# Kernel tuning notes

Measured on AMD Instinct MI355X. Metric: run time of the kernel, lower is better.

The kernel has to match this reference:

```python
import jax, jax.numpy as jnp
import numpy as np

WINDOW = 11
SIGMA = 1.5
C_IN = 3
PAD = WINDOW // 2
ALPHA_CHARB, ALPHA_MSE, ALPHA_SSIM = 0.3, 0.1, 0.6
EPS = 1e-6
C1 = (0.01 * 1) ** 2
C2 = (0.03 * 1) ** 2


def _gaussian_kernel():
    # 1D gaussian -> outer product -> depthwise weight [C, 1, K, K]
    x = np.arange(-(WINDOW // 2), WINDOW // 2 + 1, dtype=np.float32)
    w = np.exp(-0.5 * x * x / (SIGMA * SIGMA))
    w = w / w.sum()
    k2d = np.outer(w, w).astype(np.float32)  # [K, K]
    return jnp.asarray(np.tile(k2d[None, None], (C_IN, 1, 1, 1)))  # [C,1,K,K]

_KERNEL = _gaussian_kernel()


def _gauss_filter(x):
    # depthwise conv, NCHW / OIHW, SAME-style padding of K//2
    return jax.lax.conv_general_dilated(
        x, _KERNEL,
        window_strides=(1, 1),
        padding=[(PAD, PAD), (PAD, PAD)],
        dimension_numbers=('NCHW', 'OIHW', 'NCHW'),
        feature_group_count=C_IN,
    )


def setup_inputs() -> dict:
    key = jax.random.key(0)
    k1, k2 = jax.random.split(key)
    shape = (16, 3, 512, 512)
    pred = jax.random.uniform(k1, shape, dtype=jnp.float32)
    target = jax.random.uniform(k2, shape, dtype=jnp.float32)
    return {"pred": pred, "target": target}


def reference(pred, target):
    # SSIM map
    mu_x = _gauss_filter(pred)
    mu_y = _gauss_filter(target)
    sigma2_x = _gauss_filter(pred * pred) - mu_x * mu_x
    sigma2_y = _gauss_filter(target * target) - mu_y * mu_y
    sigma_xy = _gauss_filter(pred * target) - mu_x * mu_y
    A1 = 2.0 * mu_x * mu_y + C1
    A2 = 2.0 * sigma_xy + C2
    B1 = mu_x * mu_x + mu_y * mu_y + C1
    B2 = sigma2_x + sigma2_y + C2
    ssim = (A1 / B1) * (A2 / B2)

    diff = pred - target
    charb = jnp.sqrt(diff * diff + EPS * EPS)
    mse = diff * diff * 20.0
    ssim_loss = 1.0 - ssim
    return ALPHA_CHARB * charb + ALPHA_MSE * mse + ALPHA_SSIM * ssim_loss
```

## Files before the change

### kernel.cpp

```cpp
#include <hip/hip_runtime.h>


#define IMG    512
#define RAD    5
#define KW     11
#define STRH   64
#define NSTEP  (STRH + 2 * RAD)
#define ROWE   74
#define PLANE  (IMG * IMG)

#define C1F  1e-4f
#define C2F  9e-4f
#define EPS2 1e-12f

#define W0 0.00102838f
#define W1 0.00759876f
#define W2 0.03600076f
#define W3 0.10936067f
#define W4 0.21300537f
#define W5 0.26601297f

__global__ __launch_bounds__(256, 2)
void CombinedLossSSIMCharbMSE_81372450390186_kernel(
    const float* __restrict__ pred,
    const float* __restrict__ target,
    float* __restrict__ out)
{
    const float GW[KW] = {W0, W1, W2, W3, W4, W5, W4, W3, W2, W1, W0};

    __shared__ float2 rb[8 * ROWE];

    const int lane = threadIdx.x & 63;
    const int wav  = threadIdx.x >> 6;
    const int wid  = (blockIdx.x << 2) | wav;
    const int plane = wid >> 6;
    const int tile  = (wid >> 3) & 7;
    const int strip = wid & 7;
    const int col0 = strip << 6;
    const int row0 = tile << 6;
    const int pbase = plane * PLANE;

    const int  cA  = col0 - RAD + lane;
    const bool okA = (cA >= 0) & (cA < IMG);
    const int  cAc = min(max(cA, 0), IMG - 1);
    const int  cB  = col0 + 59 + lane;
    const bool okB = cB < IMG;
    const int  cBc = min(cB, IMG - 1);
    const bool doB = lane < 10;

    float hrx[KW], hry[KW], hrs[KW], hrp[KW], dring[KW];
#pragma unroll
    for (int s = 0; s < KW; ++s) {
        hrx[s] = 0.f; hry[s] = 0.f; hrs[s] = 0.f; hrp[s] = 0.f; dring[s] = 0.f;
    }

    float pAr = 0.f, tAr = 0.f, pBr = 0.f, tBr = 0.f;

#define LOAD_ROW(rr) do {                                                   \
        const int _base = pbase + (rr) * IMG;                               \
        pAr = pred[_base + cAc];   pAr = okA ? pAr : 0.f;                   \
        tAr = target[_base + cAc]; tAr = okA ? tAr : 0.f;                   \
        if (doB) {                                                          \
            pBr = pred[_base + cBc];   pBr = okB ? pBr : 0.f;               \
            tBr = target[_base + cBc]; tBr = okB ? tBr : 0.f;               \
        }                                                                   \
    } while (0)

#define COMMIT(par) do {                                                    \
        float2* _w = &rb[(((wav) << 1) | (par)) * ROWE];                    \
        _w[lane] = make_float2(pAr, tAr);                                   \
        if (doB) _w[64 + lane] = make_float2(pBr, tBr);                     \
        __builtin_amdgcn_wave_barrier();        \
    } while (0)

#define TAPS(uu, par) do {                                                  \
        const float2* _rd = &rb[(((wav) << 1) | (par)) * ROWE];             \
        float _hx = 0.f, _hy = 0.f, _hs = 0.f, _hp = 0.f;                   \
        float2 _c5 = make_float2(0.f, 0.f);                                 \
        _Pragma("unroll")                                                   \
        for (int _d = 0; _d < KW; ++_d) {                                   \
            const float2 _t = _rd[lane + _d];                               \
            if (_d == RAD) _c5 = _t;                                        \
            const float _w = GW[_d];                                        \
            _hx = fmaf(_w, _t.x, _hx);                                      \
            _hy = fmaf(_w, _t.y, _hy);                                      \
            _hs = fmaf(_w, fmaf(_t.x, _t.x, _t.y * _t.y), _hs);             \
            _hp = fmaf(_w, _t.x * _t.y, _hp);                               \
        }                                                                   \
        hrx[uu] = _hx; hry[uu] = _hy; hrs[uu] = _hs; hrp[uu] = _hp;         \
        dring[uu] = _c5.x - _c5.y;       \
    } while (0)

#define ZERO_H(uu) do {                                                     \
        hrx[uu] = 0.f; hry[uu] = 0.f; hrs[uu] = 0.f; hrp[uu] = 0.f;         \
    } while (0)

#define FINALIZE(uu, oo) do {                                               \
        float _vx = 0.f, _vy = 0.f, _vs = 0.f, _vp = 0.f;                   \
        _Pragma("unroll")                                                   \
        for (int _s = 0; _s < KW; ++_s) {                                   \
            const float _w = GW[((uu) - _s + KW) % KW];                     \
            _vx = fmaf(_w, hrx[_s], _vx);                                   \
            _vy = fmaf(_w, hry[_s], _vy);                                   \
            _vs = fmaf(_w, hrs[_s], _vs);                                   \
            _vp = fmaf(_w, hrp[_s], _vp);                                   \
        }                                                                   \
        const float _mxy = _vx * _vy;                                       \
        const float _mu2 = fmaf(_vx, _vx, _vy * _vy);                       \
        const float _A1 = fmaf(2.f, _mxy, C1F);                             \
        const float _A2 = fmaf(2.f, _vp - _mxy, C2F);                       \
        const float _B1 = _mu2 + C1F;                                       \
        const float _B2 = (_vs - _mu2) + C2F;                               \
        const float _ssim = (_A1 * _A2) * __builtin_amdgcn_rcpf(_B1 * _B2); \
        const float _dd = dring[((uu) + 6) % KW];     \
        const float _ch = __builtin_amdgcn_sqrtf(fmaf(_dd, _dd, EPS2));     \
        out[pbase + (oo) * IMG + col0 + lane] =                             \
            fmaf(0.3f, _ch, fmaf(2.0f, _dd * _dd, 0.6f * (1.f - _ssim)));   \
    } while (0)

    if (row0 > 0) LOAD_ROW(row0 - RAD);

#define STEP_PRO(uu) do {                                                   \
        const bool _inr = (row0 - RAD + (uu)) >= 0;       \
        if (_inr) COMMIT((uu) & 1);                                         \
        if ((row0 - RAD + (uu) + 1) >= 0) LOAD_ROW(row0 - RAD + (uu) + 1);  \
        if (_inr) TAPS(uu, (uu) & 1); else ZERO_H(uu);                      \
    } while (0)

    STEP_PRO(0); STEP_PRO(1); STEP_PRO(2); STEP_PRO(3); STEP_PRO(4);
    STEP_PRO(5); STEP_PRO(6); STEP_PRO(7); STEP_PRO(8); STEP_PRO(9);
    STEP_PRO(10);
    FINALIZE(10, row0);

    for (int k = 1; k <= 5; ++k) {
        const int rnext = row0 - RAD + k * KW + 1;
        const int obase = row0 + k * KW - 10;
        const int kp = k & 1;
#define STEP_FULL(uu) do {                                                  \
        COMMIT(kp ^ ((uu) & 1));                                            \
        LOAD_ROW(rnext + (uu));                                             \
        TAPS(uu, kp ^ ((uu) & 1));                                          \
        FINALIZE(uu, obase + (uu));                                         \
    } while (0)
        STEP_FULL(0); STEP_FULL(1); STEP_FULL(2); STEP_FULL(3);
        STEP_FULL(4); STEP_FULL(5); STEP_FULL(6); STEP_FULL(7);
        STEP_FULL(8); STEP_FULL(9); STEP_FULL(10);
#undef STEP_FULL
    }

#define STEP_EPI(uu) do {                                                   \
        const bool _inr = (row0 + 61 + (uu)) < IMG;       \
        if (_inr) COMMIT((uu) & 1);             \
        if (((uu) < 7) && (row0 + 62 + (uu)) < IMG)                         \
            LOAD_ROW(row0 + 62 + (uu));                                     \
        if (_inr) TAPS(uu, (uu) & 1); else ZERO_H(uu);                      \
        FINALIZE(uu, row0 + 56 + (uu));                                     \
    } while (0)

    STEP_EPI(0); STEP_EPI(1); STEP_EPI(2); STEP_EPI(3);
    STEP_EPI(4); STEP_EPI(5); STEP_EPI(6); STEP_EPI(7);
#undef STEP_EPI
#undef STEP_PRO
#undef FINALIZE
#undef ZERO_H
#undef TAPS
#undef COMMIT
#undef LOAD_ROW
}

extern "C" void kernel_launch(void* const* d_in, const int* in_sizes, int n_in,
                              void* d_out, int out_size, void* d_ws, size_t ws_size,
                              hipStream_t stream) {
    const float* pred = (const float*)d_in[0];
    const float* target = (const float*)d_in[1];
    float* out = (float*)d_out;
    const int planes = in_sizes[0] / PLANE;

    dim3 grid(planes * 16);
    CombinedLossSSIMCharbMSE_81372450390186_kernel<<<grid, dim3(256), 0, stream>>>(
        pred, target, out);
}
```

Baseline: 183.8 us.

## Prefetch input rows two steps ahead with a single LDS row buffer

Result: faster. 164.7 us (-10.4%).

```diff
diff --git a/kernel.cpp b/kernel.cpp
--- a/kernel.cpp
+++ b/kernel.cpp
@@ -5,7 +5,6 @@
 #define RAD    5
 #define KW     11
 #define STRH   64
-#define NSTEP  (STRH + 2 * RAD)
 #define ROWE   74
 #define PLANE  (IMG * IMG)
 
@@ -28,7 +27,7 @@
 {
     const float GW[KW] = {W0, W1, W2, W3, W4, W5, W4, W3, W2, W1, W0};
 
-    __shared__ float2 rb[8 * ROWE];
+    __shared__ float2 rb[4 * ROWE];
 
     const int lane = threadIdx.x & 63;
     const int wav  = threadIdx.x >> 6;
@@ -48,38 +47,41 @@
     const int  cBc = min(cB, IMG - 1);
     const bool doB = lane < 10;
 
+    const int wb = wav * ROWE;
+
     float hrx[KW], hry[KW], hrs[KW], hrp[KW], dring[KW];
 #pragma unroll
     for (int s = 0; s < KW; ++s) {
         hrx[s] = 0.f; hry[s] = 0.f; hrs[s] = 0.f; hrp[s] = 0.f; dring[s] = 0.f;
     }
 
-    float pAr = 0.f, tAr = 0.f, pBr = 0.f, tBr = 0.f;
+    float pA0 = 0.f, tA0 = 0.f, pB0 = 0.f, tB0 = 0.f;
+    float pA1 = 0.f, tA1 = 0.f, pB1 = 0.f, tB1 = 0.f;
 
-#define LOAD_ROW(rr) do {                                                   \
-        const int _base = pbase + (rr) * IMG;                               \
-        pAr = pred[_base + cAc];   pAr = okA ? pAr : 0.f;                   \
-        tAr = target[_base + cAc]; tAr = okA ? tAr : 0.f;                   \
+#define LOADR(ss, rr) do {                                                  \
+        const int _b = pbase + (rr) * IMG;                                  \
+        pA##ss = pred[_b + cAc];                                            \
+        tA##ss = target[_b + cAc];                                          \
         if (doB) {                                                          \
-            pBr = pred[_base + cBc];   pBr = okB ? pBr : 0.f;               \
-            tBr = target[_base + cBc]; tBr = okB ? tBr : 0.f;               \
+            pB##ss = pred[_b + cBc];                                        \
+            tB##ss = target[_b + cBc];                                      \
         }                                                                   \
     } while (0)
 
-#define COMMIT(par) do {                                                    \
-        float2* _w = &rb[(((wav) << 1) | (par)) * ROWE];                    \
-        _w[lane] = make_float2(pAr, tAr);                                   \
-        if (doB) _w[64 + lane] = make_float2(pBr, tBr);                     \
+#define COMMITR(ss) do {                                                    \
+        rb[wb + lane] =                                                     \
+            make_float2(okA ? pA##ss : 0.f, okA ? tA##ss : 0.f);            \
+        if (doB) rb[wb + 64 + lane] =                                       \
+            make_float2(okB ? pB##ss : 0.f, okB ? tB##ss : 0.f);            \
         __builtin_amdgcn_wave_barrier();        \
     } while (0)
 
-#define TAPS(uu, par) do {                                                  \
-        const float2* _rd = &rb[(((wav) << 1) | (par)) * ROWE];             \
+#define TAPS(uu) do {                                                       \
         float _hx = 0.f, _hy = 0.f, _hs = 0.f, _hp = 0.f;                   \
         float2 _c5 = make_float2(0.f, 0.f);                                 \
         _Pragma("unroll")                                                   \
         for (int _d = 0; _d < KW; ++_d) {                                   \
-            const float2 _t = _rd[lane + _d];                               \
+            const float2 _t = rb[wb + lane + _d];                           \
             if (_d == RAD) _c5 = _t;                                        \
             const float _w = GW[_d];                                        \
             _hx = fmaf(_w, _t.x, _hx);                                      \
@@ -118,54 +120,69 @@
             fmaf(0.3f, _ch, fmaf(2.0f, _dd * _dd, 0.6f * (1.f - _ssim)));   \
     } while (0)
 
-    if (row0 > 0) LOAD_ROW(row0 - RAD);
+    if (row0 > 0) { LOADR(0, row0 - 5); LOADR(1, row0 - 4); }
 
-#define STEP_PRO(uu) do {                                                   \
+#define STEP_PRO(uu, ss) do {                                               \
         const bool _inr = (row0 - RAD + (uu)) >= 0;       \
-        if (_inr) COMMIT((uu) & 1);                                         \
-        if ((row0 - RAD + (uu) + 1) >= 0) LOAD_ROW(row0 - RAD + (uu) + 1);  \
-        if (_inr) TAPS(uu, (uu) & 1); else ZERO_H(uu);                      \
+        if (_inr) COMMITR(ss);                                              \
+        if ((row0 - 3 + (uu)) >= 0) LOADR(ss, row0 - 3 + (uu));             \
+        if (_inr) TAPS(uu); else ZERO_H(uu);                                \
     } while (0)
 
-    STEP_PRO(0); STEP_PRO(1); STEP_PRO(2); STEP_PRO(3); STEP_PRO(4);
-    STEP_PRO(5); STEP_PRO(6); STEP_PRO(7); STEP_PRO(8); STEP_PRO(9);
-    STEP_PRO(10);
+    STEP_PRO(0, 0); STEP_PRO(1, 1); STEP_PRO(2, 0); STEP_PRO(3, 1);
+    STEP_PRO(4, 0); STEP_PRO(5, 1); STEP_PRO(6, 0); STEP_PRO(7, 1);
+    STEP_PRO(8, 0); STEP_PRO(9, 1); STEP_PRO(10, 0);
     FINALIZE(10, row0);
 
-    for (int k = 1; k <= 5; ++k) {
-        const int rnext = row0 - RAD + k * KW + 1;
-        const int obase = row0 + k * KW - 10;
-        const int kp = k & 1;
-#define STEP_FULL(uu) do {                                                  \
-        COMMIT(kp ^ ((uu) & 1));                                            \
-        LOAD_ROW(rnext + (uu));                                             \
-        TAPS(uu, kp ^ ((uu) & 1));                                          \
-        FINALIZE(uu, obase + (uu));                                         \
+#define STEP_A(m, ss) do {                                                  \
+        COMMITR(ss);                                                        \
+        LOADR(ss, row0 + 8 + (m));                                          \
+        TAPS(m);                                                            \
+        FINALIZE(m, row0 + 1 + (m));                                        \
     } while (0)
-        STEP_FULL(0); STEP_FULL(1); STEP_FULL(2); STEP_FULL(3);
-        STEP_FULL(4); STEP_FULL(5); STEP_FULL(6); STEP_FULL(7);
-        STEP_FULL(8); STEP_FULL(9); STEP_FULL(10);
-#undef STEP_FULL
+
+    STEP_A(0, 1); STEP_A(1, 0); STEP_A(2, 1); STEP_A(3, 0); STEP_A(4, 1);
+    STEP_A(5, 0); STEP_A(6, 1); STEP_A(7, 0); STEP_A(8, 1); STEP_A(9, 0);
+    STEP_A(10, 1);
+#undef STEP_A
+
+    for (int j = 0; j < 2; ++j) {
+        const int rbase = row0 + 17 + 22 * j;
+#define STEP_I(t, uu, ss) do {                                              \
+        COMMITR(ss);                                                        \
+        LOADR(ss, rbase + (t) + 2);                                         \
+        TAPS(uu);                                                           \
+        FINALIZE(uu, rbase + (t) - 5);                                      \
+    } while (0)
+        STEP_I(0, 0, 0);   STEP_I(1, 1, 1);   STEP_I(2, 2, 0);
+        STEP_I(3, 3, 1);   STEP_I(4, 4, 0);   STEP_I(5, 5, 1);
+        STEP_I(6, 6, 0);   STEP_I(7, 7, 1);   STEP_I(8, 8, 0);
+        STEP_I(9, 9, 1);   STEP_I(10, 10, 0); STEP_I(11, 0, 1);
+        STEP_I(12, 1, 0);  STEP_I(13, 2, 1);  STEP_I(14, 3, 0);
+        STEP_I(15, 4, 1);  STEP_I(16, 5, 0);  STEP_I(17, 6, 1);
+        STEP_I(18, 7, 0);  STEP_I(19, 8, 1);  STEP_I(20, 9, 0);
+        STEP_I(21, 10, 1);
+#undef STEP_I
     }
 
-#define STEP_EPI(uu) do {                                                   \
-        const bool _inr = (row0 + 61 + (uu)) < IMG;       \
-        if (_inr) COMMIT((uu) & 1);             \
-        if (((uu) < 7) && (row0 + 62 + (uu)) < IMG)                         \
-            LOAD_ROW(row0 + 62 + (uu));                                     \
-        if (_inr) TAPS(uu, (uu) & 1); else ZERO_H(uu);                      \
-        FINALIZE(uu, row0 + 56 + (uu));                                     \
+#define STEP_E(m, ss) do {                                                  \
+        const bool _inr = (row0 + 61 + (m)) < IMG;        \
+        if (_inr) COMMITR(ss);                                              \
+        if (((m) < 6) && (row0 + 63 + (m)) < IMG)                           \
+            LOADR(ss, row0 + 63 + (m));                                     \
+        if (_inr) TAPS(m); else ZERO_H(m);                                  \
+        FINALIZE(m, row0 + 56 + (m));                                       \
     } while (0)
 
-    STEP_EPI(0); STEP_EPI(1); STEP_EPI(2); STEP_EPI(3);
-    STEP_EPI(4); STEP_EPI(5); STEP_EPI(6); STEP_EPI(7);
-#undef STEP_EPI
+    STEP_E(0, 0); STEP_E(1, 1); STEP_E(2, 0); STEP_E(3, 1);
+    STEP_E(4, 0); STEP_E(5, 1); STEP_E(6, 0); STEP_E(7, 1);
+#undef STEP_E
 #undef STEP_PRO
 #undef FINALIZE
 #undef ZERO_H
 #undef TAPS
-#undef COMMIT
-#undef LOAD_ROW
+#undef COMMITR
+#undef LOADR
 }
 
 extern "C" void kernel_launch(void* const* d_in, const int* in_sizes, int n_in,
```
